# Kernel tuning notes

Hardware: AMD Instinct MI355X
Metric: run time of the kernel (lower is better)

## Reference

```python
import jax, jax.numpy as jnp
import numpy as np
import math

D_MODEL = 1024
NUM_HEADS = 16
HEAD_DIM = D_MODEL // NUM_HEADS
WINDOW = 5  # positions j with i - W//2 <= j <= i + W//2 are visible


def setup_inputs() -> dict:
    key = jax.random.key(0)
    ks = jax.random.split(key, 9)
    B, S = 2, 2048
    x = jax.random.normal(ks[0], (B, S, D_MODEL), dtype=jnp.float32)
    # Xavier-uniform linear weights [out, in] (torch convention), zero biases
    lim = math.sqrt(6.0 / (D_MODEL + D_MODEL))
    def w(k):
        return jax.random.uniform(k, (D_MODEL, D_MODEL), dtype=jnp.float32, minval=-lim, maxval=lim)
    return {
        'x': x,
        'Wq': w(ks[1]), 'bq': jnp.zeros((D_MODEL,), jnp.float32),
        'Wk': w(ks[2]), 'bk': jnp.zeros((D_MODEL,), jnp.float32),
        'Wv': w(ks[3]), 'bv': jnp.zeros((D_MODEL,), jnp.float32),
        'Wo': w(ks[4]), 'bo': jnp.zeros((D_MODEL,), jnp.float32),
    }


def reference(x, Wq, bq, Wk, bk, Wv, bv, Wo, bo):
    B, S, D = x.shape
    H, hd = NUM_HEADS, HEAD_DIM
    half = WINDOW // 2

    def proj(W, b):
        # torch Linear: y = x @ W.T + b ; split heads -> [B, H, S, hd]
        return (jnp.einsum('bsd,ed->bse', x, W) + b).reshape(B, S, H, hd).transpose(0, 2, 1, 3)

    q = proj(Wq, bq)
    k = proj(Wk, bk)
    v = proj(Wv, bv)

    scores = jnp.einsum('bhqd,bhkd->bhqk', q, k) / jnp.sqrt(jnp.asarray(hd, x.dtype))
    i = jnp.arange(S)[:, None]
    j = jnp.arange(S)[None, :]
    band = (j >= i - half) & (j <= i + half)  # [S, S] local window mask
    scores = jnp.where(band, scores, jnp.asarray(-1e9, x.dtype))
    attn = jax.nn.softmax(scores, axis=-1)  # dropout is identity in eval mode
    out = jnp.einsum('bhqk,bhkd->bhqd', attn, v)
    out = out.transpose(0, 2, 1, 3).reshape(B, S, D)
    return jnp.einsum('bsd,ed->bse', out, Wo) + bo
```

## Files before the change

kernel.cpp:

```cpp
#include <hip/hip_runtime.h>
#include <hip/hip_bf16.h>

typedef __bf16 bf16_t;
typedef __bf16 bf16x4 __attribute__((ext_vector_type(4)));
typedef __bf16 bf16x8 __attribute__((ext_vector_type(8)));
typedef float f32x4 __attribute__((ext_vector_type(4)));

#define S_LEN 2048
#define DMODEL 1024
#define NHEADS 16
#define HDIM 64
#define BROWS 4096
#define QKVN 3072

__device__ __forceinline__ void async16(const void* g, void* l) {
  __builtin_amdgcn_global_load_lds(
      (const __attribute__((address_space(1))) void*)g,
      (__attribute__((address_space(3))) void*)l, 16, 0, 0);
}

__global__ __launch_bounds__(256) void cvt_all_kernel(
    const float* __restrict__ x, const float* __restrict__ Wq,
    const float* __restrict__ Wk, const float* __restrict__ Wv,
    const float* __restrict__ Wo, bf16_t* __restrict__ dst) {
  const int i = blockIdx.x * 256 + threadIdx.x;
  constexpr int XN4 = (BROWS * DMODEL) / 4;
  constexpr int WN4 = (DMODEL * DMODEL) / 4;
  const float* src;
  size_t off;
  if (i < XN4) {
    src = x;
    off = (size_t)i;
  } else {
    const int wi = i - XN4;
    const int w = wi >> 18;
    off = (size_t)(wi & (WN4 - 1));
    src = (w == 0) ? Wq : (w == 1) ? Wk : (w == 2) ? Wv : Wo;
  }
  const float4 v = *(const float4*)(src + off * 4);
  bf16x4 o;
  o[0] = (bf16_t)v.x;
  o[1] = (bf16_t)v.y;
  o[2] = (bf16_t)v.z;
  o[3] = (bf16_t)v.w;
  *(bf16x4*)(dst + (size_t)i * 4) = o;
}

#define BARR __builtin_amdgcn_s_barrier()
#define SB0 __builtin_amdgcn_sched_barrier(0)
#define VMC3 asm volatile("s_waitcnt vmcnt(3)" ::: "memory")
#define VMC0 asm volatile("s_waitcnt vmcnt(0)" ::: "memory")

__global__ __launch_bounds__(512, 2) void gemm_qkv256_kernel(
    const bf16_t* __restrict__ A, const bf16_t* __restrict__ W,
    const float* __restrict__ bq, const float* __restrict__ bk,
    const float* __restrict__ bv, bf16_t* __restrict__ C) {
  constexpr int Kd = 1024;
  __shared__ char lds[114688];
  char* ldsA = lds;
  char* ldsB = lds + 65536;

  const int m0 = blockIdx.x * 256;
  const int n0 = blockIdx.y * 192;

  const int tid = threadIdx.x;
  const int lane = tid & 63;
  const int wid = tid >> 6;
  const int wr = wid >> 2;
  const int wc = wid & 3;
  const int fr = lane & 15;
  const int l16 = lane >> 4;

  f32x4 acc[8][3] = {};
  bf16x8 aS0[4][2], aS1[4][2], bB[3][2];

  auto stageA = [&](int buf, int h, int kt) {
#pragma unroll
    for (int l = 0; l < 2; ++l) {
      const int idx = l * 512 + tid;
      const int r = idx >> 3;
      const int slot = idx & 7;
      async16((const char*)(A + (size_t)(m0 + h * 128 + r) * Kd + kt * 64 +
                            ((slot ^ (r & 7)) << 3)),
              ldsA + buf * 32768 + h * 16384 + r * 128 + slot * 16);
    }
  };
  auto stageB = [&](int buf, int th, int kt) {
    const int r = tid >> 3;
    const int slot = tid & 7;
    async16((const char*)(W + (size_t)(n0 + th * 64 + r) * Kd + kt * 64 +
                          ((slot ^ (r & 7)) << 3)),
            ldsB + buf * 24576 + th * 8192 + r * 128 + slot * 16);
  };

  auto rdA = [&](int buf, int row, int ks) -> bf16x8 {
    return *(const bf16x8*)(ldsA + buf * 32768 + row * 128 +
                            ((((ks << 2) + l16) ^ (row & 7)) << 4));
  };
  auto rdB = [&](int buf, int row, int ks) -> bf16x8 {
    return *(const bf16x8*)(ldsB + buf * 24576 + row * 128 +
                            ((((ks << 2) + l16) ^ (row & 7)) << 4));
  };

#define RDA_TO(AS, MH, BUF)                                              \
  _Pragma("unroll") for (int m_ = 0; m_ < 4; ++m_)                       \
      _Pragma("unroll") for (int ks_ = 0; ks_ < 2; ++ks_) AS[m_][ks_] =  \
          rdA(BUF, wr * 128 + (MH)*64 + m_ * 16 + fr, ks_);
#define RDB(NF0, NC, BUF)                                                \
  _Pragma("unroll") for (int n_ = 0; n_ < (NC); ++n_)                    \
      _Pragma("unroll") for (int ks_ = 0; ks_ < 2; ++ks_)                \
          bB[(NF0) + n_][ks_] =                                          \
              rdB(BUF, wc * 48 + ((NF0) + n_) * 16 + fr, ks_);
#define MMAQ(AS, MH, NF0, NC)                                                 \
  _Pragma("unroll") for (int m_ = 0; m_ < 4; ++m_)                            \
      _Pragma("unroll") for (int n_ = 0; n_ < (NC); ++n_) {                   \
    acc[(MH)*4 + m_][(NF0) + n_] = __builtin_amdgcn_mfma_f32_16x16x32_bf16(   \
        AS[m_][0], bB[(NF0) + n_][0], acc[(MH)*4 + m_][(NF0) + n_], 0, 0, 0); \
    acc[(MH)*4 + m_][(NF0) + n_] = __builtin_amdgcn_mfma_f32_16x16x32_bf16(   \
        AS[m_][1], bB[(NF0) + n_][1], acc[(MH)*4 + m_][(NF0) + n_], 0, 0, 0); \
  }

  stageA(0, 0, 0);
  stageA(0, 1, 0);
  stageB(0, 0, 0);
  stageB(0, 1, 0);
  stageB(0, 2, 0);
  stageB(1, 0, 1);
  stageB(1, 1, 1);
  stageB(1, 2, 1);
  VMC3;
  BARR;
  RDA_TO(aS0, 0, 0);

#pragma unroll 1
  for (int i = 0; i < 8; ++i) {
    const int t0 = 2 * i, t1 = 2 * i + 1;
    const bool st = (i < 7);
    RDB(0, 2, 0);
    RDA_TO(aS1, 1, 0);
    stageA(1, 0, t1);
    SB0;
    BARR;
    __builtin_amdgcn_s_setprio(1);
    MMAQ(aS0, 0, 0, 2);
    __builtin_amdgcn_s_setprio(0);
    BARR;
    RDB(2, 1, 0);
    stageA(1, 1, t1);
    SB0;
    BARR;
    __builtin_amdgcn_s_setprio(1);
    MMAQ(aS0, 0, 2, 1);
    __builtin_amdgcn_s_setprio(0);
    BARR;
    if (st) stageB(0, 0, t0 + 2);
    SB0;
    BARR;
    __builtin_amdgcn_s_setprio(1);
    MMAQ(aS1, 1, 0, 2);
    __builtin_amdgcn_s_setprio(0);
    BARR;
    if (st) {
      stageB(0, 1, t0 + 2);
      stageB(0, 2, t0 + 2);
    }
    SB0;
    __builtin_amdgcn_s_setprio(1);
    MMAQ(aS1, 1, 2, 1);
    __builtin_amdgcn_s_setprio(0);
    SB0;
    if (st) {
      VMC3;
    } else {
      VMC0;
    }
    RDA_TO(aS0, 0, 1);
    SB0;
    BARR;
    RDB(0, 2, 1);
    RDA_TO(aS1, 1, 1);
    if (st) stageA(0, 0, t0 + 2);
    SB0;
    BARR;
    __builtin_amdgcn_s_setprio(1);
    MMAQ(aS0, 0, 0, 2);
    __builtin_amdgcn_s_setprio(0);
    BARR;
    RDB(2, 1, 1);
    if (st) stageA(0, 1, t0 + 2);
    SB0;
    BARR;
    __builtin_amdgcn_s_setprio(1);
    MMAQ(aS0, 0, 2, 1);
    __builtin_amdgcn_s_setprio(0);
    BARR;
    if (st) stageB(1, 0, t1 + 2);
    SB0;
    BARR;
    __builtin_amdgcn_s_setprio(1);
    MMAQ(aS1, 1, 0, 2);
    __builtin_amdgcn_s_setprio(0);
    BARR;
    if (st) {
      stageB(1, 1, t1 + 2);
      stageB(1, 2, t1 + 2);
    }
    SB0;
    __builtin_amdgcn_s_setprio(1);
    MMAQ(aS1, 1, 2, 1);
    __builtin_amdgcn_s_setprio(0);
    SB0;
    if (st) {
      VMC3;
      RDA_TO(aS0, 0, 0);
    }
    SB0;
    BARR;
  }
#undef RDA_TO
#undef RDB
#undef MMAQ

  const int cr = l16 * 4;
#pragma unroll
  for (int nf = 0; nf < 3; ++nf) {
    const int col = n0 + wc * 48 + nf * 16 + fr;
    const int mat = col >> 10;
    const float* bp = (mat == 0) ? bq : (mat == 1) ? bk : bv;
    const float bval = bp[col & 1023];
#pragma unroll
    for (int mf = 0; mf < 8; ++mf) {
      const int row = m0 + wr * 128 + mf * 16 + cr;
#pragma unroll
      for (int r = 0; r < 4; ++r)
        C[(size_t)(row + r) * QKVN + col] = (bf16_t)(acc[mf][nf][r] + bval);
    }
  }
}

template <typename OutT>
__device__ __forceinline__ void gemm_body(
    const bf16_t* __restrict__ A, const bf16_t* __restrict__ W,
    const float* __restrict__ bias, OutT* __restrict__ C, int m0, int n0) {
  constexpr int Kd = 1024, Nd = 1024, BK = 32, NT = Kd / BK;
  __shared__ bf16_t ldsA[2][128 * BK];
  __shared__ bf16_t ldsB[2][128 * BK];

  const int tid = threadIdx.x;
  const int lane = tid & 63;
  const int wave = tid >> 6;
  const int wr = wave >> 1;
  const int wc = wave & 1;

  f32x4 acc[4][4] = {};

  const int fr = lane & 15;
  const int ko = (lane >> 4) * 8;

  auto stage = [&](int buf, int t) {
    const int k0 = t * BK;
#pragma unroll
    for (int p = 0; p < 2; ++p) {
      const int off = (p * 256 + tid) * 16;
      const int row = off >> 6;
      const int kb = off & 63;
      async16((const char*)(A + (size_t)(m0 + row) * Kd + k0) + kb,
              (char*)ldsA[buf] + off);
      async16((const char*)(W + (size_t)(n0 + row) * Kd + k0) + kb,
              (char*)ldsB[buf] + off);
    }
  };

  auto compute = [&](int buf) {
    bf16x8 af[4], bfr[4];
#pragma unroll
    for (int i = 0; i < 4; ++i)
      af[i] = *(const bf16x8*)(ldsA[buf] + (wr * 64 + i * 16 + fr) * BK + ko);
#pragma unroll
    for (int j = 0; j < 4; ++j)
      bfr[j] = *(const bf16x8*)(ldsB[buf] + (wc * 64 + j * 16 + fr) * BK + ko);
#pragma unroll
    for (int i = 0; i < 4; ++i)
#pragma unroll
      for (int j = 0; j < 4; ++j)
        acc[i][j] = __builtin_amdgcn_mfma_f32_16x16x32_bf16(af[i], bfr[j],
                                                            acc[i][j], 0, 0, 0);
  };

  stage(0, 0);
  __syncthreads();
#pragma unroll 1
  for (int t = 0; t < NT; ++t) {
    if (t + 1 < NT) stage((t + 1) & 1, t + 1);
    compute(t & 1);
    __syncthreads();
  }

  const int cr = (lane >> 4) * 4;
#pragma unroll
  for (int j = 0; j < 4; ++j) {
    const int col = n0 + wc * 64 + j * 16 + fr;
    const float bval = bias[col];
#pragma unroll
    for (int i = 0; i < 4; ++i) {
#pragma unroll
      for (int r = 0; r < 4; ++r) {
        const int row = m0 + wr * 64 + i * 16 + cr + r;
        C[(size_t)row * Nd + col] = (OutT)(acc[i][j][r] + bval);
      }
    }
  }
}

__global__ __launch_bounds__(256) void gemm_o_kernel(
    const bf16_t* __restrict__ ctx, const bf16_t* __restrict__ Wob,
    const float* __restrict__ bo, float* __restrict__ out) {
  gemm_body<float>(ctx, Wob, bo, out, blockIdx.x * 128, blockIdx.y * 128);
}

#define CHUNK 256
#define TROWS 260

__global__ __launch_bounds__(256) void attn_kernel(
    const bf16_t* __restrict__ QKV, bf16_t* __restrict__ ctx) {
  __shared__ bf16_t ldsK[TROWS * HDIM];
  __shared__ bf16_t ldsV[TROWS * HDIM];

  const int tid = threadIdx.x;
  const int blk = blockIdx.x;
  const int chunk = blk & 7;
  const int bh = blk >> 3;
  const int h = bh & (NHEADS - 1);
  const int b = bh >> 4;
  const int s0 = chunk * CHUNK;

  const bf16_t* Kb = QKV + (size_t)b * S_LEN * QKVN + DMODEL + h * HDIM;
  const bf16_t* Vb = QKV + (size_t)b * S_LEN * QKVN + 2 * DMODEL + h * HDIM;

#pragma unroll
  for (int j = 0; j < 9; ++j) {
    const int i = j * 256 + tid;
    if (i < TROWS * 8) {
      const int tr = i >> 3;
      const int slot = i & 7;
      const int c = slot ^ (tr & 7);
      int gs = s0 - 2 + tr;
      gs = (gs < 0) ? 0 : (gs >= S_LEN ? S_LEN - 1 : gs);
      async16((const char*)(Kb + (size_t)gs * QKVN) + c * 16,
              (char*)ldsK + i * 16);
      async16((const char*)(Vb + (size_t)gs * QKVN) + c * 16,
              (char*)ldsV + i * 16);
    }
  }

  const int s = s0 + tid;
  const bf16_t* Qrow = QKV + ((size_t)(b * S_LEN) + s) * QKVN + h * HDIM;
  bf16x8 q8[8];
#pragma unroll
  for (int c = 0; c < 8; ++c) q8[c] = *(const bf16x8*)(Qrow + c * 8);
  float qf[64];
#pragma unroll
  for (int c = 0; c < 8; ++c)
#pragma unroll
    for (int e = 0; e < 8; ++e) qf[c * 8 + e] = (float)q8[c][e];

  __syncthreads();

  float sc[5];
#pragma unroll
  for (int jj = 0; jj < 5; ++jj) {
    const int tr = tid + jj;
    float d = 0.f;
#pragma unroll
    for (int c = 0; c < 8; ++c) {
      const bf16x8 k8 = *(const bf16x8*)(ldsK + tr * HDIM + (c ^ (tr & 7)) * 8);
#pragma unroll
      for (int e = 0; e < 8; ++e) d += qf[c * 8 + e] * (float)k8[e];
    }
    const int j = s - 2 + jj;
    sc[jj] = (j < 0 || j >= S_LEN) ? -1e30f : d * 0.125f;
  }

  float m = sc[0];
#pragma unroll
  for (int jj = 1; jj < 5; ++jj) m = fmaxf(m, sc[jj]);
  float p[5], l = 0.f;
#pragma unroll
  for (int jj = 0; jj < 5; ++jj) {
    p[jj] = __expf(sc[jj] - m);
    l += p[jj];
  }
  const float inv = 1.0f / l;
#pragma unroll
  for (int jj = 0; jj < 5; ++jj) p[jj] *= inv;

  float o[64];
#pragma unroll
  for (int e = 0; e < 64; ++e) o[e] = 0.f;
#pragma unroll
  for (int jj = 0; jj < 5; ++jj) {
    const int tr = tid + jj;
    const float pj = p[jj];
#pragma unroll
    for (int c = 0; c < 8; ++c) {
      const bf16x8 v8 = *(const bf16x8*)(ldsV + tr * HDIM + (c ^ (tr & 7)) * 8);
#pragma unroll
      for (int e = 0; e < 8; ++e) o[c * 8 + e] += pj * (float)v8[e];
    }
  }

  bf16_t* Crow = (bf16_t*)ctx + ((size_t)(b * S_LEN) + s) * DMODEL + h * HDIM;
#pragma unroll
  for (int c = 0; c < 8; ++c) {
    bf16x8 ov;
#pragma unroll
    for (int e = 0; e < 8; ++e) ov[e] = (bf16_t)o[c * 8 + e];
    *(bf16x8*)(Crow + c * 8) = ov;
  }
}

extern "C" void kernel_launch(void* const* d_in, const int* in_sizes, int n_in,
                              void* d_out, int out_size, void* d_ws,
                              size_t ws_size, hipStream_t stream) {
  const float* x = (const float*)d_in[0];
  const float* Wq = (const float*)d_in[1];
  const float* bq = (const float*)d_in[2];
  const float* Wk = (const float*)d_in[3];
  const float* bk = (const float*)d_in[4];
  const float* Wv = (const float*)d_in[5];
  const float* bv = (const float*)d_in[6];
  const float* Wo = (const float*)d_in[7];
  const float* bo = (const float*)d_in[8];
  float* out = (float*)d_out;

  const size_t mat = (size_t)BROWS * DMODEL;
  const size_t wmat = (size_t)DMODEL * DMODEL;
  bf16_t* xb = (bf16_t*)d_ws;
  bf16_t* Wqkv = xb + mat;
  bf16_t* Wob = Wqkv + 3 * wmat;
  bf16_t* QKV = Wob + wmat;
  bf16_t* ctx = QKV + 3 * mat;

  cvt_all_kernel<<<8192, 256, 0, stream>>>(x, Wq, Wk, Wv, Wo, xb);

  gemm_qkv256_kernel<<<dim3(16, 16), 512, 0, stream>>>(xb, Wqkv, bq, bk, bv,
                                                       QKV);
  attn_kernel<<<256, 256, 0, stream>>>(QKV, ctx);
  gemm_o_kernel<<<dim3(32, 8), 256, 0, stream>>>(ctx, Wob, bo, out);
}
```

Baseline: 77.92 us.

## Use 512-thread blocks for output GEMM and restructure QKV loop A-fragment reads

The output-projection GEMM now runs with 8 waves per 128x128 tile in a 2x4 layout, so each wave computes 64x32 and each thread issues one async load per matrix per stage. This aims to add latency hiding and waves per CU for a GEMM with only 256 blocks. Separately, in the QKV GEMM loop the first A-fragment LDS read moves to the top of each iteration, and a barrier replaces the waitcnt/barrier pair before the second half. This may cost some prefetch overlap across iterations.

```diff
diff --git a/kernel.cpp b/kernel.cpp
--- a/kernel.cpp
+++ b/kernel.cpp
@@ -130,12 +130,12 @@
   stageB(1, 2, 1);
   VMC3;
   BARR;
-  RDA_TO(aS0, 0, 0);
 
 #pragma unroll 1
   for (int i = 0; i < 8; ++i) {
     const int t0 = 2 * i, t1 = 2 * i + 1;
     const bool st = (i < 7);
+    RDA_TO(aS0, 0, 0);
     RDB(0, 2, 0);
     RDA_TO(aS1, 1, 0);
     stageA(1, 0, t1);
@@ -174,9 +174,8 @@
     } else {
       VMC0;
     }
+    BARR;
     RDA_TO(aS0, 0, 1);
-    SB0;
-    BARR;
     RDB(0, 2, 1);
     RDA_TO(aS1, 1, 1);
     if (st) stageA(0, 0, t0 + 2);
@@ -210,11 +209,7 @@
     MMAQ(aS1, 1, 2, 1);
     __builtin_amdgcn_s_setprio(0);
     SB0;
-    if (st) {
-      VMC3;
-      RDA_TO(aS0, 0, 0);
-    }
-    SB0;
+    if (st) VMC3;
     BARR;
   }
 #undef RDA_TO
@@ -238,52 +233,49 @@
   }
 }
 
-template <typename OutT>
-__device__ __forceinline__ void gemm_body(
-    const bf16_t* __restrict__ A, const bf16_t* __restrict__ W,
-    const float* __restrict__ bias, OutT* __restrict__ C, int m0, int n0) {
+__global__ __launch_bounds__(512) void gemm_o_kernel(
+    const bf16_t* __restrict__ Adat, const bf16_t* __restrict__ W,
+    const float* __restrict__ bias, float* __restrict__ out) {
   constexpr int Kd = 1024, Nd = 1024, BK = 32, NT = Kd / BK;
   __shared__ bf16_t ldsA[2][128 * BK];
   __shared__ bf16_t ldsB[2][128 * BK];
 
+  const int m0 = blockIdx.x * 128;
+  const int n0 = blockIdx.y * 128;
+
   const int tid = threadIdx.x;
   const int lane = tid & 63;
-  const int wave = tid >> 6;
-  const int wr = wave >> 1;
-  const int wc = wave & 1;
-
-  f32x4 acc[4][4] = {};
-
+  const int wid = tid >> 6;
+  const int wr = wid >> 2;
+  const int wc = wid & 3;
   const int fr = lane & 15;
   const int ko = (lane >> 4) * 8;
 
+  f32x4 acc[4][2] = {};
+
   auto stage = [&](int buf, int t) {
     const int k0 = t * BK;
-#pragma unroll
-    for (int p = 0; p < 2; ++p) {
-      const int off = (p * 256 + tid) * 16;
-      const int row = off >> 6;
-      const int kb = off & 63;
-      async16((const char*)(A + (size_t)(m0 + row) * Kd + k0) + kb,
-              (char*)ldsA[buf] + off);
-      async16((const char*)(W + (size_t)(n0 + row) * Kd + k0) + kb,
-              (char*)ldsB[buf] + off);
-    }
+    const int row = tid >> 2;
+    const int kb = (tid & 3) * 16;
+    async16((const char*)(Adat + (size_t)(m0 + row) * Kd + k0) + kb,
+            (char*)ldsA[buf] + row * 64 + kb);
+    async16((const char*)(W + (size_t)(n0 + row) * Kd + k0) + kb,
+            (char*)ldsB[buf] + row * 64 + kb);
   };
 
   auto compute = [&](int buf) {
-    bf16x8 af[4], bfr[4];
+    bf16x8 af[4], bf[2];
 #pragma unroll
     for (int i = 0; i < 4; ++i)
       af[i] = *(const bf16x8*)(ldsA[buf] + (wr * 64 + i * 16 + fr) * BK + ko);
 #pragma unroll
-    for (int j = 0; j < 4; ++j)
-      bfr[j] = *(const bf16x8*)(ldsB[buf] + (wc * 64 + j * 16 + fr) * BK + ko);
+    for (int j = 0; j < 2; ++j)
+      bf[j] = *(const bf16x8*)(ldsB[buf] + (wc * 32 + j * 16 + fr) * BK + ko);
 #pragma unroll
     for (int i = 0; i < 4; ++i)
 #pragma unroll
-      for (int j = 0; j < 4; ++j)
-        acc[i][j] = __builtin_amdgcn_mfma_f32_16x16x32_bf16(af[i], bfr[j],
+      for (int j = 0; j < 2; ++j)
+        acc[i][j] = __builtin_amdgcn_mfma_f32_16x16x32_bf16(af[i], bf[j],
                                                             acc[i][j], 0, 0, 0);
   };
 
@@ -298,24 +290,18 @@
 
   const int cr = (lane >> 4) * 4;
 #pragma unroll
-  for (int j = 0; j < 4; ++j) {
-    const int col = n0 + wc * 64 + j * 16 + fr;
+  for (int j = 0; j < 2; ++j) {
+    const int col = n0 + wc * 32 + j * 16 + fr;
     const float bval = bias[col];
 #pragma unroll
     for (int i = 0; i < 4; ++i) {
 #pragma unroll
       for (int r = 0; r < 4; ++r) {
         const int row = m0 + wr * 64 + i * 16 + cr + r;
-        C[(size_t)row * Nd + col] = (OutT)(acc[i][j][r] + bval);
+        out[(size_t)row * Nd + col] = acc[i][j][r] + bval;
       }
     }
   }
-}
-
-__global__ __launch_bounds__(256) void gemm_o_kernel(
-    const bf16_t* __restrict__ ctx, const bf16_t* __restrict__ Wob,
-    const float* __restrict__ bo, float* __restrict__ out) {
-  gemm_body<float>(ctx, Wob, bo, out, blockIdx.x * 128, blockIdx.y * 128);
 }
 
 #define CHUNK 256
@@ -442,9 +428,8 @@
   bf16_t* ctx = QKV + 3 * mat;
 
   cvt_all_kernel<<<8192, 256, 0, stream>>>(x, Wq, Wk, Wv, Wo, xb);
-
   gemm_qkv256_kernel<<<dim3(16, 16), 512, 0, stream>>>(xb, Wqkv, bq, bk, bv,
                                                        QKV);
   attn_kernel<<<256, 256, 0, stream>>>(QKV, ctx);
-  gemm_o_kernel<<<dim3(32, 8), 256, 0, stream>>>(ctx, Wob, bo, out);
-}
+  gemm_o_kernel<<<dim3(32, 8), 512, 0, stream>>>(ctx, Wob, bo, out);
+}
```

Result: no change. 78.20 us (+0.4%).
